# Kernel optimization log

Measured on AMD Instinct MI355X. Metric: run time of the kernel, lower is better.

The kernel has to match this reference:

```python
import jax, jax.numpy as jnp
import numpy as np

N_EMB = 256
HEAD_SIZE = 64
B, S = 4, 4096


def setup_inputs() -> dict:
    key = jax.random.key(0)
    k1, k2, k3, k4 = jax.random.split(key, 4)
    return {
        "ini_emb": jax.random.normal(k1, (B, S, N_EMB), dtype=jnp.float32),
        "wk": jax.random.normal(k2, (N_EMB, HEAD_SIZE), dtype=jnp.float32) * (N_EMB ** -0.5),
        "wq": jax.random.normal(k3, (N_EMB, HEAD_SIZE), dtype=jnp.float32) * (N_EMB ** -0.5),
        "wv": jax.random.normal(k4, (N_EMB, HEAD_SIZE), dtype=jnp.float32) * (N_EMB ** -0.5),
    }


def reference(ini_emb, wk, wq, wv):
    # projections: [B,S,E] @ [E,H] -> [B,S,H]
    k = ini_emb @ wk
    q = ini_emb @ wq
    v = ini_emb @ wv
    # scores: [B,S,S]; NOTE: source scales by n_emb**-0.5, not head_size**-0.5
    scores = jnp.einsum("bqh,bkh->bqk", q, k) * (N_EMB ** -0.5)
    attn = jax.nn.softmax(scores, axis=-1)
    # output: [B,S,H]
    return jnp.einsum("bqk,bkh->bqh", attn, v)
```

## Files before the change

kernel.cpp:

```cpp
#include <hip/hip_runtime.h>


typedef short short4v __attribute__((ext_vector_type(4)));
typedef short short8v __attribute__((ext_vector_type(8)));
typedef unsigned short ushort8v __attribute__((ext_vector_type(8)));
typedef float floatx4 __attribute__((ext_vector_type(4)));
typedef unsigned short u16;
typedef unsigned int u32;

#define SEQ 4096
#define EMB 256
#define HD 64
#define PADA 264

static __device__ __forceinline__ u16 f2bf(float x) {
    union { float f; unsigned u; } v; v.f = x;
    unsigned r = v.u + 0x7FFFu + ((v.u >> 16) & 1u);
    return (u16)(r >> 16);
}

static __device__ __forceinline__ u32 cvt_pk_bf16(float a, float b) {
    u32 r;
    asm("v_cvt_pk_bf16_f32 %0, %1, %2" : "=v"(r) : "v"(a), "v"(b));
    return r;
}

static __device__ __forceinline__ short4v pack_bf4(float a, float b, float c, float d) {
    union { u32 u[2]; short4v s; } x;
    x.u[0] = cvt_pk_bf16(a, b);
    x.u[1] = cvt_pk_bf16(c, d);
    return x.s;
}

__global__ __launch_bounds__(256) void prep_w(
    const float* __restrict__ wk, const float* __restrict__ wq, const float* __restrict__ wv,
    u16* __restrict__ wt) {
    const int nt = blockIdx.x;
    const int t = threadIdx.x;
#pragma unroll
    for (int ss = 0; ss < 2; ++ss) {
        int slot = t + ss * 256;
        int kc = slot >> 6, lane = slot & 63;
        int ln15 = lane & 15, lq = lane >> 4;
        int cg = nt * 16 + ln15;
        int mat = cg >> 6, col = cg & 63;
        const float* W = (mat == 0) ? wq : (mat == 1) ? wk : wv;
        const float s = (mat == 0) ? 0.0625f * 1.44269504088896f : 1.0f;
        u32 w4[4];
#pragma unroll
        for (int p = 0; p < 2; ++p) {
#pragma unroll
            for (int d = 0; d < 2; ++d) {
                int e0 = kc * 32 + lq * 8 + p * 4 + d * 2;
                u16 lo = f2bf(W[(e0 + 0) * HD + col] * s);
                u16 hi = f2bf(W[(e0 + 1) * HD + col] * s);
                w4[p * 2 + d] = (u32)lo | ((u32)hi << 16);
            }
        }
        u32* dst = (u32*)wt + ((size_t)(nt * 8 + kc) * 64 + lane) * 4;
        *(uint4*)dst = make_uint4(w4[0], w4[1], w4[2], w4[3]);
    }
}

__global__ __launch_bounds__(256) void proj_mfma(
    const float* __restrict__ emb, const u16* __restrict__ wt,
    u16* __restrict__ qb, u16* __restrict__ kb, u16* __restrict__ vbt) {
    __shared__ u16 a_s[32 * PADA];
    __shared__ __align__(16) u16 ot_s[12][32][16];
    const int t = threadIdx.x;
    const int lane = t & 63;
    const int wave = t >> 6;
    const int ln15 = lane & 15;
    const int lq = lane >> 4;
    const size_t row0 = (size_t)blockIdx.x * 32;

#pragma unroll
    for (int c = 0; c < 8; ++c) {
        int f = t + c * 256;
        int row = f >> 6, e4 = (f & 63) * 4;
        float4 v = *(const float4*)(emb + (row0 + row) * EMB + e4);
        u32 lo = cvt_pk_bf16(v.x, v.y);
        u32 hi = cvt_pk_bf16(v.z, v.w);
        *(uint2*)&a_s[row * PADA + e4] = make_uint2(lo, hi);
    }
    __syncthreads();

    floatx4 acc[2][3];
#pragma unroll
    for (int rg = 0; rg < 2; ++rg)
#pragma unroll
        for (int j = 0; j < 3; ++j) {
            floatx4 z = { 0.f, 0.f, 0.f, 0.f };
            acc[rg][j] = z;
        }

#pragma unroll
    for (int kc = 0; kc < 8; ++kc) {
        short8v a0 = *(const short8v*)&a_s[ln15 * PADA + kc * 32 + lq * 8];
        short8v a1 = *(const short8v*)&a_s[(16 + ln15) * PADA + kc * 32 + lq * 8];
#pragma unroll
        for (int j = 0; j < 3; ++j) {
            short8v b = *(const short8v*)(wt + (((size_t)(wave * 3 + j) * 8 + kc) * 64 + lane) * 8);
            acc[0][j] = __builtin_amdgcn_mfma_f32_16x16x32_bf16(a0, b, acc[0][j], 0, 0, 0);
            acc[1][j] = __builtin_amdgcn_mfma_f32_16x16x32_bf16(a1, b, acc[1][j], 0, 0, 0);
        }
    }

#pragma unroll
    for (int rg = 0; rg < 2; ++rg)
#pragma unroll
        for (int j = 0; j < 3; ++j)
#pragma unroll
            for (int r = 0; r < 4; ++r)
                ot_s[wave * 3 + j][rg * 16 + lq * 4 + r][ln15] = f2bf(acc[rg][j][r]);
    __syncthreads();

    {
        const int row = t >> 3, chunk = t & 7;
        const int tile = chunk >> 1, off = (chunk & 1) * 8;
        ushort8v qv = *(const ushort8v*)&ot_s[tile][row][off];
        *(ushort8v*)&qb[(row0 + row) * HD + chunk * 8] = qv;
        ushort8v kv = *(const ushort8v*)&ot_s[4 + tile][row][off];
        *(ushort8v*)&kb[(row0 + row) * HD + chunk * 8] = kv;
    }
    {
        const int h = t >> 2, sc = t & 3;
        const int tile = 8 + (h >> 4), tcol = h & 15;
        union { u16 u[8]; ushort8v v; } g;
#pragma unroll
        for (int i = 0; i < 8; ++i)
            g.u[i] = ot_s[tile][sc * 8 + i][tcol];
        size_t bidx = row0 >> 12;
        size_t sl = (row0 & 4095) + sc * 8;
        *(ushort8v*)&vbt[(bidx * 64 + h) * SEQ + sl] = g.v;
    }
}


__global__ __launch_bounds__(256) void attn_kernel(
    const u16* __restrict__ qb, const u16* __restrict__ kb, const u16* __restrict__ vbt,
    float* __restrict__ po, float* __restrict__ pml) {
    __shared__ __align__(16) u16 smem[4][64 * 64];

    const int t = threadIdx.x;
    const int lane = t & 63;
    const int wave = t >> 6;
    const int ln15 = lane & 15;
    const int lq = lane >> 4;

    const int part = ((blockIdx.x & 7) << 6) | (blockIdx.x >> 3);
    const int b = part >> 7;
    const int qblk = (part >> 2) & 31;
    const int split = part & 3;
    const int q0 = qblk * 128;

    const u16* __restrict__ qpb = qb + ((size_t)b * SEQ + q0) * HD;
    const u16* __restrict__ kpb = kb + (size_t)b * SEQ * HD;
    const u16* __restrict__ vpb = vbt + (size_t)b * HD * SEQ;

    short8v qf[2][2];
#pragma unroll
    for (int nt = 0; nt < 2; ++nt)
#pragma unroll
        for (int h = 0; h < 2; ++h)
            qf[nt][h] = *(const short8v*)(qpb + (size_t)(wave * 32 + nt * 16 + ln15) * HD + h * 32 + lq * 8);

    floatx4 oacc[4][2];
#pragma unroll
    for (int ht = 0; ht < 4; ++ht)
#pragma unroll
        for (int nt = 0; nt < 2; ++nt) {
            floatx4 z = { 0.f, 0.f, 0.f, 0.f };
            oacc[ht][nt] = z;
        }
    float lacc[2] = { 0.f, 0.f };

    const int r0 = t >> 3, c0 = t & 7, r1 = r0 + 32;
    const int sw0 = r0 * 64 + ((c0 ^ (r0 & 7)) * 8);
    const int sw1 = r1 * 64 + ((c0 ^ (r1 & 7)) * 8);

    const int xk = ln15 & 7;
    const int ksw_lo = ln15 * 64 + ((lq ^ xk) * 8);
    const int ksw_hi = ln15 * 64 + (((4 + lq) ^ xk) * 8);
    const int vch0 = lq >> 1, vsub = (lq & 1) * 4;

    uint4 ka, kb4, va, vb4;
    {
        const int kwb = (split * 16) * 64;
        ka  = *(const uint4*)(kpb + (size_t)(kwb + r0) * HD + c0 * 8);
        kb4 = *(const uint4*)(kpb + (size_t)(kwb + r1) * HD + c0 * 8);
        va  = *(const uint4*)(vpb + (size_t)r0 * SEQ + kwb + c0 * 8);
        vb4 = *(const uint4*)(vpb + (size_t)r1 * SEQ + kwb + c0 * 8);
        *(uint4*)(&smem[0][0] + sw0) = ka;
        *(uint4*)(&smem[0][0] + sw1) = kb4;
        *(uint4*)(&smem[1][0] + sw0) = va;
        *(uint4*)(&smem[1][0] + sw1) = vb4;
    }
    __syncthreads();

#pragma unroll 1
    for (int tt = 0; tt < 16; ++tt) {
        const int buf = tt & 1;
        if (tt < 15) {
            const int kwb = (split * 16 + tt + 1) * 64;
            ka  = *(const uint4*)(kpb + (size_t)(kwb + r0) * HD + c0 * 8);
            kb4 = *(const uint4*)(kpb + (size_t)(kwb + r1) * HD + c0 * 8);
            va  = *(const uint4*)(vpb + (size_t)r0 * SEQ + kwb + c0 * 8);
            vb4 = *(const uint4*)(vpb + (size_t)r1 * SEQ + kwb + c0 * 8);
        }

        const u16* ktp = &smem[buf * 2 + 0][0];
        const u16* vtp = &smem[buf * 2 + 1][0];

#pragma unroll
        for (int kt = 0; kt < 4; ++kt) {
            short8v k0 = *(const short8v*)(ktp + kt * 1024 + ksw_lo);
            short8v k1 = *(const short8v*)(ktp + kt * 1024 + ksw_hi);

            floatx4 s[2];
            __builtin_amdgcn_s_setprio(1);
#pragma unroll
            for (int nt = 0; nt < 2; ++nt) {
                floatx4 z = { 0.f, 0.f, 0.f, 0.f };
                s[nt] = __builtin_amdgcn_mfma_f32_16x16x32_bf16(k0, qf[nt][0], z, 0, 0, 0);
                s[nt] = __builtin_amdgcn_mfma_f32_16x16x32_bf16(k1, qf[nt][1], s[nt], 0, 0, 0);
            }
            __builtin_amdgcn_s_setprio(0);

            short4v pf[2];
#pragma unroll
            for (int nt = 0; nt < 2; ++nt) {
                float p0 = __builtin_amdgcn_exp2f(s[nt][0]);
                float p1 = __builtin_amdgcn_exp2f(s[nt][1]);
                float p2 = __builtin_amdgcn_exp2f(s[nt][2]);
                float p3 = __builtin_amdgcn_exp2f(s[nt][3]);
                lacc[nt] += (p0 + p1) + (p2 + p3);
                pf[nt] = pack_bf4(p0, p1, p2, p3);
            }

            __builtin_amdgcn_s_setprio(1);
#pragma unroll
            for (int ht = 0; ht < 4; ++ht) {
                short4v vf = *(const short4v*)(vtp + ht * 1024 + ln15 * 64
                               + (((kt * 2 + vch0) ^ xk) * 8) + vsub);
#pragma unroll
                for (int nt = 0; nt < 2; ++nt)
                    oacc[ht][nt] = __builtin_amdgcn_mfma_f32_16x16x16bf16_1k(
                        vf, pf[nt], oacc[ht][nt], 0, 0, 0);
            }
            __builtin_amdgcn_s_setprio(0);
        }

        if (tt < 15) {
            u16* ktn = &smem[(buf ^ 1) * 2 + 0][0];
            u16* vtn = &smem[(buf ^ 1) * 2 + 1][0];
            *(uint4*)(ktn + sw0) = ka;
            *(uint4*)(ktn + sw1) = kb4;
            *(uint4*)(vtn + sw0) = va;
            *(uint4*)(vtn + sw1) = vb4;
        }
        __syncthreads();
    }

#pragma unroll
    for (int nt = 0; nt < 2; ++nt) {
        lacc[nt] += __shfl_xor(lacc[nt], 16);
        lacc[nt] += __shfl_xor(lacc[nt], 32);
    }
    if (lq == 0) {
#pragma unroll
        for (int nt = 0; nt < 2; ++nt)
            pml[(size_t)part * 128 + wave * 32 + nt * 16 + ln15] = lacc[nt];
    }

    float* __restrict__ pob = po + (size_t)part * 8192;
#pragma unroll
    for (int ht = 0; ht < 4; ++ht)
#pragma unroll
        for (int nt = 0; nt < 2; ++nt)
            *(floatx4*)&pob[(wave * 32 + nt * 16 + ln15) * 64 + ht * 16 + lq * 4] = oacc[ht][nt];
}

__global__ __launch_bounds__(256) void reduce_kernel(
    const float* __restrict__ po, const float* __restrict__ pml,
    float* __restrict__ out) {
    __shared__ float ls[128];
    const int t = threadIdx.x;
    const int bq = blockIdx.x >> 1;
    const int half = blockIdx.x & 1;
    const int part0 = bq * 4;

    if (t < 128)
        ls[t] = pml[(size_t)(part0 + 0) * 128 + t] + pml[(size_t)(part0 + 1) * 128 + t]
              + pml[(size_t)(part0 + 2) * 128 + t] + pml[(size_t)(part0 + 3) * 128 + t];
    __syncthreads();

    const float* __restrict__ p0 = po + (size_t)(part0 + 0) * 8192;
    const float* __restrict__ p1 = po + (size_t)(part0 + 1) * 8192;
    const float* __restrict__ p2 = po + (size_t)(part0 + 2) * 8192;
    const float* __restrict__ p3 = po + (size_t)(part0 + 3) * 8192;
    float* __restrict__ ob = out + ((size_t)(bq >> 5) * SEQ + (size_t)(bq & 31) * 128) * HD;

#pragma unroll
    for (int i = 0; i < 4; ++i) {
        int f4 = half * 1024 + t + i * 256;
        int f = f4 * 4;
        int q = f4 >> 4;
        float4 a = *(const float4*)&p0[f];
        float4 c = *(const float4*)&p1[f];
        float4 d = *(const float4*)&p2[f];
        float4 e = *(const float4*)&p3[f];
        float inv = 1.0f / ls[q];
        float4 r;
        r.x = (a.x + c.x + d.x + e.x) * inv;
        r.y = (a.y + c.y + d.y + e.y) * inv;
        r.z = (a.z + c.z + d.z + e.z) * inv;
        r.w = (a.w + c.w + d.w + e.w) * inv;
        *(float4*)&ob[f] = r;
    }
}

extern "C" void kernel_launch(void* const* d_in, const int* in_sizes, int n_in,
                              void* d_out, int out_size, void* d_ws, size_t ws_size,
                              hipStream_t stream) {
    const float* emb = (const float*)d_in[0];
    const float* wk  = (const float*)d_in[1];
    const float* wq  = (const float*)d_in[2];
    const float* wv  = (const float*)d_in[3];

    u16* qb  = (u16*)d_ws;
    u16* kb  = (u16*)((char*)d_ws + (size_t)2 * 1024 * 1024);
    u16* vbt = (u16*)((char*)d_ws + (size_t)4 * 1024 * 1024);
    u16* wt  = (u16*)((char*)d_ws + (size_t)6 * 1024 * 1024);
    float* po  = (float*)((char*)d_ws + (size_t)6 * 1024 * 1024 + 256 * 1024);
    float* pml = (float*)((char*)d_ws + (size_t)22 * 1024 * 1024 + 256 * 1024);
    float* out = (float*)d_out;

    prep_w<<<12, 256, 0, stream>>>(wk, wq, wv, wt);
    proj_mfma<<<512, 256, 0, stream>>>(emb, wt, qb, kb, vbt);
    attn_kernel<<<512, 256, 0, stream>>>(qb, kb, vbt, po, pml);
    reduce_kernel<<<256, 256, 0, stream>>>(po, pml, out);
}
```

Baseline: 112.3 us.

## Fuse split-KV reduction into attention kernel via last-block atomic counter

Removes the separate reduce kernel launch. Each attention block bumps a per-query-block atomic counter after writing its partial output and row sums. The fourth block to finish combines the four partials and writes the normalized output. This saves a launch and the gap between kernels, at the cost of threadfences, an atomic per block, and serial reduction work on the last block of each group. Counters are zeroed in prep_w.

After: 179.8 us. 1.6x slower.

```diff
diff --git a/kernel.cpp b/kernel.cpp
--- a/kernel.cpp
+++ b/kernel.cpp
@@ -34,9 +34,10 @@
 
 __global__ __launch_bounds__(256) void prep_w(
     const float* __restrict__ wk, const float* __restrict__ wq, const float* __restrict__ wv,
-    u16* __restrict__ wt) {
+    u16* __restrict__ wt, u32* __restrict__ cnt) {
     const int nt = blockIdx.x;
     const int t = threadIdx.x;
+    if (nt == 0 && t < 128) cnt[t] = 0;
 #pragma unroll
     for (int ss = 0; ss < 2; ++ss) {
         int slot = t + ss * 256;
@@ -139,8 +140,11 @@
 
 __global__ __launch_bounds__(256) void attn_kernel(
     const u16* __restrict__ qb, const u16* __restrict__ kb, const u16* __restrict__ vbt,
-    float* __restrict__ po, float* __restrict__ pml) {
+    float* __restrict__ po, float* __restrict__ pml,
+    u32* __restrict__ cnt, float* __restrict__ out) {
     __shared__ __align__(16) u16 smem[4][64 * 64];
+    __shared__ float ls[128];
+    __shared__ u32 amLast;
 
     const int t = threadIdx.x;
     const int lane = t & 63;
@@ -153,6 +157,7 @@
     const int qblk = (part >> 2) & 31;
     const int split = part & 3;
     const int q0 = qblk * 128;
+    const int bq = part >> 2;
 
     const u16* __restrict__ qpb = qb + ((size_t)b * SEQ + q0) * HD;
     const u16* __restrict__ kpb = kb + (size_t)b * SEQ * HD;
@@ -279,17 +284,18 @@
 #pragma unroll
         for (int nt = 0; nt < 2; ++nt)
             *(floatx4*)&pob[(wave * 32 + nt * 16 + ln15) * 64 + ht * 16 + lq * 4] = oacc[ht][nt];
-}
-
-__global__ __launch_bounds__(256) void reduce_kernel(
-    const float* __restrict__ po, const float* __restrict__ pml,
-    float* __restrict__ out) {
-    __shared__ float ls[128];
-    const int t = threadIdx.x;
-    const int bq = blockIdx.x >> 1;
-    const int half = blockIdx.x & 1;
+
+    __threadfence();
+    __syncthreads();
+    if (t == 0) {
+        u32 old = atomicAdd(&cnt[bq], 1u);
+        amLast = (old == 3u);
+    }
+    __syncthreads();
+    if (!amLast) return;
+    __threadfence();
+
     const int part0 = bq * 4;
-
     if (t < 128)
         ls[t] = pml[(size_t)(part0 + 0) * 128 + t] + pml[(size_t)(part0 + 1) * 128 + t]
               + pml[(size_t)(part0 + 2) * 128 + t] + pml[(size_t)(part0 + 3) * 128 + t];
@@ -299,11 +305,11 @@
     const float* __restrict__ p1 = po + (size_t)(part0 + 1) * 8192;
     const float* __restrict__ p2 = po + (size_t)(part0 + 2) * 8192;
     const float* __restrict__ p3 = po + (size_t)(part0 + 3) * 8192;
-    float* __restrict__ ob = out + ((size_t)(bq >> 5) * SEQ + (size_t)(bq & 31) * 128) * HD;
-
-#pragma unroll
-    for (int i = 0; i < 4; ++i) {
-        int f4 = half * 1024 + t + i * 256;
+    float* __restrict__ ob = out + ((size_t)b * SEQ + (size_t)qblk * 128) * HD;
+
+#pragma unroll
+    for (int i = 0; i < 8; ++i) {
+        int f4 = t + i * 256;
         int f = f4 * 4;
         int q = f4 >> 4;
         float4 a = *(const float4*)&p0[f];
@@ -334,10 +340,10 @@
     u16* wt  = (u16*)((char*)d_ws + (size_t)6 * 1024 * 1024);
     float* po  = (float*)((char*)d_ws + (size_t)6 * 1024 * 1024 + 256 * 1024);
     float* pml = (float*)((char*)d_ws + (size_t)22 * 1024 * 1024 + 256 * 1024);
+    u32* cnt = (u32*)((char*)d_ws + (size_t)23 * 1024 * 1024);
     float* out = (float*)d_out;
 
-    prep_w<<<12, 256, 0, stream>>>(wk, wq, wv, wt);
+    prep_w<<<12, 256, 0, stream>>>(wk, wq, wv, wt, cnt);
     proj_mfma<<<512, 256, 0, stream>>>(emb, wt, qb, kb, vbt);
-    attn_kernel<<<512, 256, 0, stream>>>(qb, kb, vbt, po, pml);
-    reduce_kernel<<<256, 256, 0, stream>>>(po, pml, out);
-}
+    attn_kernel<<<512, 256, 0, stream>>>(qb, kb, vbt, po, pml, cnt, out);
+}
```
